# Kernel tuning notes

Hardware: AMD Instinct MI355X
Metric: run time of the kernel (lower is better)

The kernel has to match this reference:

```python
import jax, jax.numpy as jnp
from jax import lax
import numpy as np

DN = ('NCHW', 'OIHW', 'NCHW')

def conv(x, w, b, stride, pad):
    y = lax.conv_general_dilated(x, w, (stride, stride), [(pad, pad), (pad, pad)], dimension_numbers=DN)
    return y if b is None else y + b[None, :, None, None]

def conv_transpose(x, w, b):
    # torch ConvTranspose2d(k=4, s=2, p=1); w in torch layout (Cin, Cout, 4, 4)
    w_f = jnp.flip(w, (2, 3)).transpose(1, 0, 2, 3)  # -> OIHW, flipped
    y = lax.conv_general_dilated(x, w_f, (1, 1), [(2, 2), (2, 2)], lhs_dilation=(2, 2), dimension_numbers=DN)
    return y + b[None, :, None, None]

def res_stack(x, w3, w1, n_layers=2):
    # shared weights across layers (ModuleList([layer]*n) aliases one module)
    for _ in range(n_layers):
        h = conv(jax.nn.relu(x), w3, None, 1, 1)
        h = conv(jax.nn.relu(h), w1, None, 1, 0)
        x = x + h
    return jax.nn.relu(x)

def setup_inputs() -> dict:
    key = jax.random.key(0)
    ks = jax.random.split(key, 16)
    s = 0.02
    d = {
        'x': jax.random.normal(ks[0], (32, 3, 256, 256), jnp.float32),
        'enc_w1': jax.random.normal(ks[1], (128, 3, 4, 4), jnp.float32) * s,
        'enc_b1': jnp.zeros((128,), jnp.float32),
        'enc_w2': jax.random.normal(ks[2], (256, 128, 4, 4), jnp.float32) * s,
        'enc_b2': jnp.zeros((256,), jnp.float32),
        'enc_w3': jax.random.normal(ks[3], (512, 256, 4, 4), jnp.float32) * s,
        'enc_b3': jnp.zeros((512,), jnp.float32),
        'enc_res_w3': jax.random.normal(ks[4], (32, 512, 3, 3), jnp.float32) * s,
        'enc_res_w1': jax.random.normal(ks[5], (512, 32, 1, 1), jnp.float32) * s,
        'prevq_w': jax.random.normal(ks[6], (64, 512, 1, 1), jnp.float32) * s,
        'prevq_b': jnp.zeros((64,), jnp.float32),
        'emb': jax.random.normal(ks[7], (512, 64), jnp.float32),
        'dec_w1': jax.random.normal(ks[8], (64, 256, 4, 4), jnp.float32) * s,
        'dec_b1': jnp.zeros((256,), jnp.float32),
        'dec_res_w3': jax.random.normal(ks[9], (32, 256, 3, 3), jnp.float32) * s,
        'dec_res_w1': jax.random.normal(ks[10], (256, 32, 1, 1), jnp.float32) * s,
        'dec_w2': jax.random.normal(ks[11], (256, 128, 4, 4), jnp.float32) * s,
        'dec_b2': jnp.zeros((128,), jnp.float32),
        'dec_w3': jax.random.normal(ks[12], (128, 3, 4, 4), jnp.float32) * s,
        'dec_b3': jnp.zeros((3,), jnp.float32),
    }
    return d

def vqvae_fwd(x, enc_w1, enc_b1, enc_w2, enc_b2, enc_w3, enc_b3, enc_res_w3, enc_res_w1,
              prevq_w, prevq_b, emb, dec_w1, dec_b1, dec_res_w3, dec_res_w1,
              dec_w2, dec_b2, dec_w3, dec_b3):
    # encoder
    z = jax.nn.relu(conv(x, enc_w1, enc_b1, 2, 1))
    z = jax.nn.relu(conv(z, enc_w2, enc_b2, 2, 1))
    z = conv(z, enc_w3, enc_b3, 2, 1)
    z = res_stack(z, enc_res_w3, enc_res_w1)
    z_e = conv(z, prevq_w, prevq_b, 1, 0)  # (B, D=64, 32, 32)
    # vector quantiser
    B, C, H, W = z_e.shape
    x_flat = z_e.reshape(B, C, H * W).transpose(0, 2, 1)  # (B, HW, D)
    d2 = (jnp.sum(x_flat ** 2, -1, keepdims=True)
          - 2.0 * jnp.einsum('bnd,kd->bnk', x_flat, emb)
          + jnp.sum(emb ** 2, -1))
    idx = jnp.argmin(d2, axis=2)  # (B, HW)
    z_q_flat = emb[idx]  # (B, HW, D)
    z_q = z_q_flat.transpose(0, 2, 1).reshape(B, C, H, W)
    sg = lax.stop_gradient
    q_loss = jnp.mean((sg(z_q_flat) - x_flat) ** 2) + jnp.mean((z_q_flat - sg(x_flat)) ** 2)
    # decoder
    y = conv_transpose(z_q, dec_w1, dec_b1)  # (B, 256, 64, 64)
    y = res_stack(y, dec_res_w3, dec_res_w1)
    y = jax.nn.relu(conv_transpose(y, dec_w2, dec_b2))
    y = conv_transpose(y, dec_w3, dec_b3)  # (B, 3, 256, 256)
    return y, q_loss

def reference(x, enc_w1, enc_b1, enc_w2, enc_b2, enc_w3, enc_b3, enc_res_w3, enc_res_w1,
              prevq_w, prevq_b, emb, dec_w1, dec_b1, dec_res_w3, dec_res_w1,
              dec_w2, dec_b2, dec_w3, dec_b3):
    return vqvae_fwd(x, enc_w1, enc_b1, enc_w2, enc_b2, enc_w3, enc_b3, enc_res_w3, enc_res_w1,
                     prevq_w, prevq_b, emb, dec_w1, dec_b1, dec_res_w3, dec_res_w1,
                     dec_w2, dec_b2, dec_w3, dec_b3)
```

## Files before the change

### kernel.cpp

```cpp
#include <hip/hip_runtime.h>
#include <hip/hip_bf16.h>

typedef __attribute__((ext_vector_type(8))) short short8;
typedef __attribute__((ext_vector_type(4))) float f32x4;
typedef __attribute__((ext_vector_type(4))) unsigned int uint4v;

__device__ __forceinline__ unsigned short f2bf(float f) {
  unsigned u = __builtin_bit_cast(unsigned, f);
  u = (u + 0x7FFFu + ((u >> 16) & 1u)) >> 16;
  return (unsigned short)u;
}
__device__ __forceinline__ float bf2f(unsigned short h) {
  unsigned u = ((unsigned)h) << 16;
  return __builtin_bit_cast(float, u);
}
__device__ __forceinline__ unsigned pk_bf16(float a, float b) {
  __hip_bfloat162 h = __float22bfloat162_rn(make_float2(a, b));
  unsigned u;
  __builtin_memcpy(&u, &h, 4);
  return u;
}

template<int TMT, int MT, int MODE, int ZSP, bool SPLIT, bool RELU_IN, bool RELU_OUT, bool BIAS, int SM>
__global__ __launch_bounds__(256, (MT == 4) ? 3 : 4) void k_mfconv(
    const float* __restrict__ in, const unsigned short* __restrict__ wp,
    const float* __restrict__ bias, float* __restrict__ out,
    int Ci, int inW, int inH, int pWSH, int pHWSH,
    int Co, int ntap, int ntt,
    unsigned syp, unsigned sxp,
    int outW, int outHW, int CoSt) {
  const int tid  = threadIdx.x;
  const int lane = tid & 63, wave = tid >> 6;
  const int pW  = 1 << pWSH;
  const int pHW = 1 << pHWSH;
  const int inHW = inW * inH;
  const int nk32 = Ci >> 5;
  const int KS   = (nk32 >= 2) ? 2 : 1;
  const int NITS = 4 * KS;
  const int cpt  = nk32 / KS;
  const int total = ntap * cpt;
  constexpr int TT = TMT * MT;

  int bx = blockIdx.x;
  const int gx = gridDim.x;
  if ((gx & 7) == 0) bx = (bx & 7) * (gx >> 3) + (bx >> 3);
  const int n0  = bx * 64;
  const int coG = blockIdx.y;
  const int ph  = (MODE == 1) ? blockIdx.z : 0;
  const int tap0 = (MODE == 1) ? ph * 4 : 0;
  const int pdy = ph >> 1, pdx = ph & 1;

  int it0 = 0, itEnd = total;
  if (MODE != 1 && ZSP > 1) {
    const int per = total / ZSP;
    it0 = blockIdx.z * per;
    itEnd = it0 + per;
  }

  constexpr int NPL = SPLIT ? 2 : 1;
  constexpr int PL = 64 * 70;
  __shared__ __align__(16) unsigned short Bs[2 * NPL * PL];

  const int px  = lane;
  const int p   = n0 + px;
  const int img = p >> pHWSH;
  const int rem = p & (pHW - 1);
  const int y   = rem >> pWSH;
  const int x   = rem & (pW - 1);
  const size_t base_img = (size_t)img * Ci * inHW;

  constexpr int NTO = (TMT == 4) ? 4 : 2;
  const int mt0 = (TMT == 4) ? wave : (wave & 1);
  const int ntb = (TMT == 4) ? 0 : ((wave >> 1) * 2);
  f32x4 acc[MT * NTO];
#pragma unroll
  for (int u = 0; u < MT * NTO; ++u) acc[u] = (f32x4){0.f, 0.f, 0.f, 0.f};

  const int cp = wave;
  float v[16];

  auto ldr = [&](int tap_, int chunk_) {
    const int T = tap0 + tap_;
    const int dy = (int)((syp >> (2 * T)) & 3u) - 1;
    const int dx = (int)((sxp >> (2 * T)) & 3u) - 1;
    const int ys = (MODE == 2) ? (2 * y + dy) : (y + dy);
    const int xs = (MODE == 2) ? (2 * x + dx) : (x + dx);
    const bool ok = ((unsigned)ys < (unsigned)inH) && ((unsigned)xs < (unsigned)inW);
    const float* __restrict__ ipb = in + base_img + (ptrdiff_t)ys * inW + xs;
    const int ci0 = chunk_ * (KS * 32);
#pragma unroll
    for (int it2 = 0; it2 < 8; ++it2) {
      if (it2 >= NITS) break;
      const int cl = 2 * (cp + 4 * it2);
      float a = 0.f, b = 0.f;
      if (ok) {
        a = ipb[(size_t)(ci0 + cl) * inHW];
        b = ipb[(size_t)(ci0 + cl + 1) * inHW];
      }
      if (RELU_IN) { a = fmaxf(a, 0.f); b = fmaxf(b, 0.f); }
      v[2 * it2] = a; v[2 * it2 + 1] = b;
    }
  };
  auto pwr = [&](int b) {
#pragma unroll
    for (int it2 = 0; it2 < 8; ++it2) {
      if (it2 >= NITS) break;
      const int cl = 2 * (cp + 4 * it2);
      float a = v[2 * it2], c = v[2 * it2 + 1];
      unsigned hp = pk_bf16(a, c);
      *(unsigned*)&Bs[(b * NPL) * PL + px * 70 + cl] = hp;
      if (SPLIT) {
        float h0 = bf2f((unsigned short)hp), h1 = bf2f((unsigned short)(hp >> 16));
        *(unsigned*)&Bs[(b * NPL + 1) * PL + px * 70 + cl] = pk_bf16(a - h0, c - h1);
      }
    }
  };

  int tap = it0 / cpt, chunk = it0 % cpt;
  ldr(tap, chunk);
  pwr(0);
  __syncthreads();

  for (int it = it0; it < itEnd; ++it) {
    const int b = (it - it0) & 1;
    const int T = tap0 + tap;
    int tap2 = tap, chunk2 = chunk + 1;
    if (chunk2 == cpt) { chunk2 = 0; tap2 = tap + 1; }
    const bool more = (it + 1 < itEnd);
    if (more) ldr(tap2, chunk2);
#pragma unroll
    for (int s = 0; s < 2; ++s) {
      if (s >= KS) break;
      const int cic = chunk * KS + s;
      short8 ah[MT], al[MT];
#pragma unroll
      for (int m = 0; m < MT; ++m) {
        const int mtm = mt0 + m * TMT;
        size_t abase;
        if (SPLIT) abase = ((((size_t)coG * ntt + T) * nk32 + cic) * 2 * TT + mtm) * 512;
        else       abase = ((((size_t)coG * ntt + T) * nk32 + cic) * TT + mtm) * 512;
        ah[m] = *(const short8*)(wp + abase + (size_t)lane * 8);
        if (SPLIT) al[m] = *(const short8*)(wp + abase + (size_t)TT * 512 + (size_t)lane * 8);
      }
      short8 bh[NTO], bl[NTO];
#pragma unroll
      for (int u = 0; u < NTO; ++u) {
        const int row = 16 * (ntb + u) + (lane & 15);
        const unsigned* bp = (const unsigned*)&Bs[(b * NPL) * PL + row * 70 + s * 32 + (lane >> 4) * 8];
        uint4v hv = {bp[0], bp[1], bp[2], bp[3]};
        bh[u] = __builtin_bit_cast(short8, hv);
        if (SPLIT) {
          const unsigned* bpl = bp + (PL >> 1);
          uint4v lv = {bpl[0], bpl[1], bpl[2], bpl[3]};
          bl[u] = __builtin_bit_cast(short8, lv);
        }
      }
#pragma unroll
      for (int m = 0; m < MT; ++m)
#pragma unroll
        for (int u = 0; u < NTO; ++u) {
          f32x4 a = acc[m * NTO + u];
          a = __builtin_amdgcn_mfma_f32_16x16x32_bf16(ah[m], bh[u], a, 0, 0, 0);
          if (SPLIT) {
            a = __builtin_amdgcn_mfma_f32_16x16x32_bf16(al[m], bh[u], a, 0, 0, 0);
            a = __builtin_amdgcn_mfma_f32_16x16x32_bf16(ah[m], bl[u], a, 0, 0, 0);
          }
          acc[m * NTO + u] = a;
        }
    }
    if (more) {
      pwr(b ^ 1);
      __syncthreads();
    }
    tap = tap2; chunk = chunk2;
  }

#pragma unroll
  for (int m = 0; m < MT; ++m) {
    const int mtm = mt0 + m * TMT;
#pragma unroll
    for (int u = 0; u < NTO; ++u) {
      const int nt = ntb + u;
      const int pn = n0 + nt * 16 + (lane & 15);
      const int img2 = pn >> pHWSH;
      const int rem2 = pn & (pHW - 1);
      const int y2 = rem2 >> pWSH, x2 = rem2 & (pW - 1);
      int oy, ox;
      if (MODE == 1) { oy = 2 * y2 + pdy; ox = 2 * x2 + pdx; }
      else           { oy = y2;           ox = x2; }
#pragma unroll
      for (int r = 0; r < 4; ++r) {
        const int co = coG * (TT * 16) + mtm * 16 + (lane >> 4) * 4 + r;
        if (co < CoSt) {
          float val = acc[m * NTO + u][r];
          if (BIAS) val += bias[co];
          if (RELU_OUT) val = fmaxf(val, 0.f);
          size_t oi = ((size_t)img2 * Co + co) * outHW + (size_t)oy * outW + ox;
          if (SM == 0) out[oi] = val;
          else if (SM == 1) out[oi] += val;
          else atomicAdd(&out[oi], val);
        }
      }
    }
  }
}

template<int MGRP, bool SPLIT>
__global__ __launch_bounds__(256, SPLIT ? 3 : 4) void k_mfres(
    const float* __restrict__ in, const unsigned short* __restrict__ w3p,
    const unsigned short* __restrict__ w1p, float* __restrict__ znew,
    int pWSH, int pHWSH, unsigned syp, unsigned sxp) {
  constexpr int C = MGRP * 64;
  const int tid = threadIdx.x, lane = tid & 63, wave = tid >> 6;
  const int pW = 1 << pWSH, pHW = 1 << pHWSH;
  const int inW = pW, inH = pHW >> pWSH;
  const int inHW = pHW;
  const int nk32 = C >> 5;
  const int cpt = nk32 >> 1;
  const int total = 9 * cpt;

  int bx = blockIdx.x;
  const int gx = gridDim.x;
  if ((gx & 7) == 0) bx = (bx & 7) * (gx >> 3) + (bx >> 3);
  const int n0 = bx * 64;

  constexpr int NPL = SPLIT ? 2 : 1;
  constexpr int PL = 64 * 70;
  __shared__ __align__(16) unsigned short Bs[2 * NPL * PL];
  __shared__ __align__(16) unsigned short Hs2[NPL * 2560];

  const int px = lane;
  const int p = n0 + px;
  const int img = p >> pHWSH;
  const int rem = p & (pHW - 1);
  const int y = rem >> pWSH, x = rem & (pW - 1);
  const size_t base_img = (size_t)img * C * inHW;
  const int mt = wave & 1, ntb = (wave >> 1) * 2;
  const int cp = wave;
  float v[16];
  f32x4 acc[2];
  acc[0] = (f32x4){0.f, 0.f, 0.f, 0.f};
  acc[1] = (f32x4){0.f, 0.f, 0.f, 0.f};

  auto ldr = [&](int T, int chunk_) {
    const int dy = (int)((syp >> (2 * T)) & 3u) - 1;
    const int dx = (int)((sxp >> (2 * T)) & 3u) - 1;
    const int ys = y + dy, xs = x + dx;
    const bool ok = ((unsigned)ys < (unsigned)inH) && ((unsigned)xs < (unsigned)inW);
    const float* __restrict__ ipb = in + base_img + (ptrdiff_t)ys * inW + xs;
    const int ci0 = chunk_ * 64;
#pragma unroll
    for (int i2 = 0; i2 < 8; ++i2) {
      const int cl = 2 * (cp + 4 * i2);
      float a = 0.f, b = 0.f;
      if (ok) {
        a = ipb[(size_t)(ci0 + cl) * inHW];
        b = ipb[(size_t)(ci0 + cl + 1) * inHW];
      }
      a = fmaxf(a, 0.f); b = fmaxf(b, 0.f);
      v[2 * i2] = a; v[2 * i2 + 1] = b;
    }
  };
  auto pwr = [&](int b) {
#pragma unroll
    for (int i2 = 0; i2 < 8; ++i2) {
      const int cl = 2 * (cp + 4 * i2);
      float a = v[2 * i2], c = v[2 * i2 + 1];
      unsigned hp = pk_bf16(a, c);
      *(unsigned*)&Bs[(b * NPL) * PL + px * 70 + cl] = hp;
      if (SPLIT) {
        float h0 = bf2f((unsigned short)hp), h1 = bf2f((unsigned short)(hp >> 16));
        *(unsigned*)&Bs[(b * NPL + 1) * PL + px * 70 + cl] = pk_bf16(a - h0, c - h1);
      }
    }
  };

  int tap = 0, chunk = 0;
  ldr(0, 0);
  pwr(0);
  __syncthreads();
  for (int it = 0; it < total; ++it) {
    const int b = it & 1;
    const int T = tap;
    int tap2 = tap, chunk2 = chunk + 1;
    if (chunk2 == cpt) { chunk2 = 0; tap2 = tap + 1; }
    const bool more = (it + 1 < total);
    if (more) ldr(tap2, chunk2);
#pragma unroll
    for (int s = 0; s < 2; ++s) {
      const int cic = chunk * 2 + s;
      size_t abase;
      if (SPLIT) abase = (((size_t)T * nk32 + cic) * 2 * 2 + mt) * 512;
      else       abase = (((size_t)T * nk32 + cic) * 2 + mt) * 512;
      short8 ah = *(const short8*)(w3p + abase + (size_t)lane * 8);
      short8 al;
      if (SPLIT) al = *(const short8*)(w3p + abase + 2 * 512 + (size_t)lane * 8);
#pragma unroll
      for (int u = 0; u < 2; ++u) {
        const int row = 16 * (ntb + u) + (lane & 15);
        const unsigned* bp = (const unsigned*)&Bs[(b * NPL) * PL + row * 70 + s * 32 + (lane >> 4) * 8];
        uint4v hv = {bp[0], bp[1], bp[2], bp[3]};
        short8 bh = __builtin_bit_cast(short8, hv);
        f32x4 a = acc[u];
        a = __builtin_amdgcn_mfma_f32_16x16x32_bf16(ah, bh, a, 0, 0, 0);
        if (SPLIT) {
          const unsigned* bpl = bp + (PL >> 1);
          uint4v lv = {bpl[0], bpl[1], bpl[2], bpl[3]};
          short8 bl = __builtin_bit_cast(short8, lv);
          a = __builtin_amdgcn_mfma_f32_16x16x32_bf16(al, bh, a, 0, 0, 0);
          a = __builtin_amdgcn_mfma_f32_16x16x32_bf16(ah, bl, a, 0, 0, 0);
        }
        acc[u] = a;
      }
    }
    if (more) {
      pwr(b ^ 1);
      __syncthreads();
    }
    tap = tap2; chunk = chunk2;
  }

#pragma unroll
  for (int u = 0; u < 2; ++u) {
    const int pxl = (ntb + u) * 16 + (lane & 15);
#pragma unroll
    for (int r = 0; r < 4; ++r) {
      const int co = mt * 16 + (lane >> 4) * 4 + r;
      float val = fmaxf(acc[u][r], 0.f);
      unsigned short hv = f2bf(val);
      Hs2[pxl * 40 + co] = hv;
      if (SPLIT) Hs2[2560 + pxl * 40 + co] = f2bf(val - bf2f(hv));
    }
  }
  __syncthreads();

  short8 bh2[4], bl2[4];
#pragma unroll
  for (int u = 0; u < 4; ++u) {
    const int row = 16 * u + (lane & 15);
    bh2[u] = *(const short8*)&Hs2[row * 40 + (lane >> 4) * 8];
    if (SPLIT) bl2[u] = *(const short8*)&Hs2[2560 + row * 40 + (lane >> 4) * 8];
  }
#pragma unroll
  for (int g = 0; g < MGRP; ++g) {
    const int mt2 = wave + 4 * g;
    short8 a1h = *(const short8*)(w1p + (size_t)mt2 * 512 + (size_t)lane * 8);
    short8 a1l;
    if (SPLIT) a1l = *(const short8*)(w1p + ((size_t)(MGRP * 4) + mt2) * 512 + (size_t)lane * 8);
    f32x4 a2[4];
#pragma unroll
    for (int u = 0; u < 4; ++u) a2[u] = (f32x4){0.f, 0.f, 0.f, 0.f};
#pragma unroll
    for (int u = 0; u < 4; ++u) {
      a2[u] = __builtin_amdgcn_mfma_f32_16x16x32_bf16(a1h, bh2[u], a2[u], 0, 0, 0);
      if (SPLIT) {
        a2[u] = __builtin_amdgcn_mfma_f32_16x16x32_bf16(a1l, bh2[u], a2[u], 0, 0, 0);
        a2[u] = __builtin_amdgcn_mfma_f32_16x16x32_bf16(a1h, bl2[u], a2[u], 0, 0, 0);
      }
    }
#pragma unroll
    for (int u = 0; u < 4; ++u) {
      const int pn = n0 + u * 16 + (lane & 15);
      const int rem2 = pn & (pHW - 1);
#pragma unroll
      for (int r = 0; r < 4; ++r) {
        const int co = mt2 * 16 + (lane >> 4) * 4 + r;
        size_t oi = ((size_t)img * C + co) * inHW + rem2;
        znew[oi] = in[oi] + a2[u][r];
      }
    }
  }
}

__global__ __launch_bounds__(256, 4) void k_mfenc1(
    const float* __restrict__ in, const unsigned short* __restrict__ wp,
    const float* __restrict__ bias, float* __restrict__ out) {
  const int tid = threadIdx.x, lane = tid & 63, wave = tid >> 6;
  int bx = blockIdx.x;
  const int gx = gridDim.x;
  if ((gx & 7) == 0) bx = (bx & 7) * (gx >> 3) + (bx >> 3);
  const int n0 = bx * 64;
  const int p = n0 + lane;
  const int img = p >> 14;
  const int rem = p & 16383;
  const int y = rem >> 7, x = rem & 127;
  __shared__ __align__(16) unsigned short Bs[2 * 4480];
  const float* __restrict__ ib = in + (size_t)img * 3 * 65536;
#pragma unroll
  for (int i = 0; i < 8; ++i) {
    const int kk0 = 2 * (wave + 4 * i);
    float vv[2];
#pragma unroll
    for (int q = 0; q < 2; ++q) {
      const int kk = kk0 + q;
      const int tap = kk >> 2, c = kk & 3;
      const int iy = 2 * y + (tap >> 2) - 1, ix = 2 * x + (tap & 3) - 1;
      const bool ok = (c < 3) && ((unsigned)iy < 256u) && ((unsigned)ix < 256u);
      vv[q] = ok ? ib[((size_t)c << 16) + (size_t)iy * 256 + ix] : 0.f;
    }
    unsigned hp = pk_bf16(vv[0], vv[1]);
    *(unsigned*)&Bs[lane * 70 + kk0] = hp;
    float h0 = bf2f((unsigned short)hp), h1 = bf2f((unsigned short)(hp >> 16));
    *(unsigned*)&Bs[4480 + lane * 70 + kk0] = pk_bf16(vv[0] - h0, vv[1] - h1);
  }
  __syncthreads();

  f32x4 acc[8];
#pragma unroll
  for (int u = 0; u < 8; ++u) acc[u] = (f32x4){0.f, 0.f, 0.f, 0.f};
#pragma unroll
  for (int s = 0; s < 2; ++s) {
    short8 ah[2], al[2];
#pragma unroll
    for (int m = 0; m < 2; ++m) {
      const int mtm = wave + m * 4;
      size_t abase = (((size_t)s * 2 + 0) * 8 + mtm) * 512;
      ah[m] = *(const short8*)(wp + abase + (size_t)lane * 8);
      al[m] = *(const short8*)(wp + abase + 8 * 512 + (size_t)lane * 8);
    }
    short8 bh[4], bl[4];
#pragma unroll
    for (int u = 0; u < 4; ++u) {
      const int row = 16 * u + (lane & 15);
      const unsigned* bp = (const unsigned*)&Bs[row * 70 + s * 32 + (lane >> 4) * 8];
      uint4v hv = {bp[0], bp[1], bp[2], bp[3]};
      bh[u] = __builtin_bit_cast(short8, hv);
      const unsigned* bpl = bp + 2240;
      uint4v lv = {bpl[0], bpl[1], bpl[2], bpl[3]};
      bl[u] = __builtin_bit_cast(short8, lv);
    }
#pragma unroll
    for (int m = 0; m < 2; ++m)
#pragma unroll
      for (int u = 0; u < 4; ++u) {
        f32x4 a = acc[m * 4 + u];
        a = __builtin_amdgcn_mfma_f32_16x16x32_bf16(ah[m], bh[u], a, 0, 0, 0);
        a = __builtin_amdgcn_mfma_f32_16x16x32_bf16(al[m], bh[u], a, 0, 0, 0);
        a = __builtin_amdgcn_mfma_f32_16x16x32_bf16(ah[m], bl[u], a, 0, 0, 0);
        acc[m * 4 + u] = a;
      }
  }
#pragma unroll
  for (int m = 0; m < 2; ++m)
#pragma unroll
    for (int u = 0; u < 4; ++u) {
      const int pn = n0 + u * 16 + (lane & 15);
      const int img2 = pn >> 14;
      const int rem2 = pn & 16383;
#pragma unroll
      for (int r = 0; r < 4; ++r) {
        const int co = (wave + m * 4) * 16 + (lane >> 4) * 4 + r;
        float val = fmaxf(acc[m * 4 + u][r] + bias[co], 0.f);
        out[((size_t)img2 * 128 + co) * 16384 + rem2] = val;
      }
    }
}

template<bool SPLIT>
__global__ __launch_bounds__(256) void k_pack_o(
    const float* __restrict__ w, unsigned short* __restrict__ p,
    int Co, int Ci, int ntap, int TMT, int E) {
  int i = blockIdx.x * 256 + threadIdx.x;
  if (i >= E) return;
  const int NC = Ci >> 5;
  int j = i & 7, lane = (i >> 3) & 63, r = i >> 9;
  int mt = r % TMT; r /= TMT;
  int sp = 0;
  if (SPLIT) { sp = r % 2; r /= 2; }
  int cic = r % NC; r /= NC;
  int T = r % ntap; int coG = r / ntap;
  int co = coG * (TMT * 16) + mt * 16 + (lane & 15);
  int ci = cic * 32 + (lane >> 4) * 8 + j;
  float wv = w[((size_t)co * Ci + ci) * ntap + T];
  unsigned short hv = f2bf(wv);
  p[i] = (SPLIT && sp == 1) ? f2bf(wv - bf2f(hv)) : hv;
}

__global__ __launch_bounds__(256) void k_pack_ct(
    const float* __restrict__ w, unsigned short* __restrict__ p,
    int Ci, int CoR, int TMT, int E) {
  int i = blockIdx.x * 256 + threadIdx.x;
  if (i >= E) return;
  const int NC = Ci >> 5;
  int j = i & 7, lane = (i >> 3) & 63, r = i >> 9;
  int mt = r % TMT; r /= TMT;
  int cic = r % NC; r /= NC;
  int T = r % 16;   int coG = r / 16;
  int phx = T >> 2, t = T & 3;
  int dy = phx >> 1, dx = phx & 1, ty = t >> 1, tx = t & 1;
  int ky = 2 * ty + 1 - dy, kx = 2 * tx + 1 - dx;
  int co = coG * (TMT * 16) + mt * 16 + (lane & 15);
  int ci = cic * 32 + (lane >> 4) * 8 + j;
  float wv = (co < CoR) ? w[(((size_t)ci * CoR + co) * 4 + ky) * 4 + kx] : 0.f;
  p[i] = f2bf(wv);
}

__global__ __launch_bounds__(256) void k_pack_e1(
    const float* __restrict__ w, unsigned short* __restrict__ p) {
  int i = blockIdx.x * 256 + threadIdx.x;
  int j = i & 7, lane = (i >> 3) & 63, r = i >> 9;
  int mt = r % 8; r /= 8;
  int sp = r % 2; r /= 2;
  int cic = r;
  int co = mt * 16 + (lane & 15);
  int kk = cic * 32 + (lane >> 4) * 8 + j;
  int tap = kk >> 2, c = kk & 3;
  float wv = (c < 3) ? w[(((size_t)co * 3 + c) * 4 + (tap >> 2)) * 4 + (tap & 3)] : 0.f;
  unsigned short hv = f2bf(wv);
  p[i] = (sp == 1) ? f2bf(wv - bf2f(hv)) : hv;
}

template<int COB, bool RELU_OUT>
__global__ __launch_bounds__(256) void k_conv4(
    const float* __restrict__ in, const float* __restrict__ w,
    const float* __restrict__ bias, float* __restrict__ out,
    int N, int Ci, int Hi, int Wi, int Co) {
  const int Ho = Hi >> 1, Wo = Wi >> 1;
  const int ow = blockIdx.x * 16 + (threadIdx.x & 15);
  const int oh = blockIdx.y * 16 + (threadIdx.x >> 4);
  const int zcnt = Co / COB;
  const int co0 = (blockIdx.z % zcnt) * COB;
  const int n   = blockIdx.z / zcnt;
  if (oh >= Ho || ow >= Wo) return;
  const float* __restrict__ ip = in + (size_t)n * Ci * Hi * Wi;
  float acc[COB];
#pragma unroll
  for (int j = 0; j < COB; ++j) acc[j] = bias[co0 + j];
  const int ih0 = 2 * oh - 1, iw0 = 2 * ow - 1;
  for (int ci = 0; ci < Ci; ++ci) {
    const float* __restrict__ ic = ip + (size_t)ci * Hi * Wi;
    float v[16];
#pragma unroll
    for (int kh = 0; kh < 4; ++kh) {
      const int ih = ih0 + kh;
      const bool hok = (unsigned)ih < (unsigned)Hi;
      const float* __restrict__ irow = ic + (long)ih * Wi;
#pragma unroll
      for (int kw = 0; kw < 4; ++kw) {
        const int iw = iw0 + kw;
        v[kh * 4 + kw] = (hok && (unsigned)iw < (unsigned)Wi) ? irow[iw] : 0.f;
      }
    }
#pragma unroll
    for (int j = 0; j < COB; ++j) {
      const float* __restrict__ wc = w + ((size_t)(co0 + j) * Ci + ci) * 16;
#pragma unroll
      for (int t = 0; t < 16; ++t) acc[j] = fmaf(v[t], wc[t], acc[j]);
    }
  }
#pragma unroll
  for (int j = 0; j < COB; ++j) {
    float a = acc[j];
    if (RELU_OUT) a = fmaxf(a, 0.f);
    out[(((size_t)n * Co + co0 + j) * Ho + oh) * Wo + ow] = a;
  }
}

template<int COB, bool RELU_IN, int CSPLIT>
__global__ __launch_bounds__(256) void k_conv3(
    const float* __restrict__ in, const float* __restrict__ w,
    float* __restrict__ out, int N, int Ci, int H, int W, int Co) {
  const int ow = blockIdx.x * 16 + (threadIdx.x & 15);
  const int oh = blockIdx.y * 16 + (threadIdx.x >> 4);
  const int zcnt = Co / COB;
  const int z = blockIdx.z;
  const int cs  = z % CSPLIT;
  const int co0 = ((z / CSPLIT) % zcnt) * COB;
  const int n   = z / (CSPLIT * zcnt);
  if (oh >= H || ow >= W) return;
  const int CPS = Ci / CSPLIT;
  const float* __restrict__ ip = in + (size_t)n * Ci * H * W;
  float acc[COB];
#pragma unroll
  for (int j = 0; j < COB; ++j) acc[j] = 0.f;
  for (int ci = cs * CPS; ci < (cs + 1) * CPS; ++ci) {
    const float* __restrict__ ic = ip + (size_t)ci * H * W;
    float v[9];
#pragma unroll
    for (int kh = 0; kh < 3; ++kh) {
      const int ih = oh - 1 + kh;
      const bool hok = (unsigned)ih < (unsigned)H;
      const float* __restrict__ irow = ic + (long)ih * W;
#pragma unroll
      for (int kw = 0; kw < 3; ++kw) {
        const int iw = ow - 1 + kw;
        float t = (hok && (unsigned)iw < (unsigned)W) ? irow[iw] : 0.f;
        if (RELU_IN) t = fmaxf(t, 0.f);
        v[kh * 3 + kw] = t;
      }
    }
#pragma unroll
    for (int j = 0; j < COB; ++j) {
      const float* __restrict__ wc = w + ((size_t)(co0 + j) * Ci + ci) * 9;
#pragma unroll
      for (int t = 0; t < 9; ++t) acc[j] = fmaf(v[t], wc[t], acc[j]);
    }
  }
#pragma unroll
  for (int j = 0; j < COB; ++j) {
    size_t oi = (((size_t)n * Co + co0 + j) * H + oh) * W + ow;
    if (CSPLIT > 1) atomicAdd(&out[oi], acc[j]);
    else out[oi] = acc[j];
  }
}

template<int COB, bool RELU_IN, bool ACCUM>
__global__ __launch_bounds__(256) void k_conv1(
    const float* __restrict__ in, const float* __restrict__ w,
    const float* __restrict__ bias, float* __restrict__ out,
    int N, int Ci, int P, int Co) {
  const int p = blockIdx.x * 256 + threadIdx.x;
  const int co0 = blockIdx.y * COB;
  const int n = blockIdx.z;
  if (p >= P) return;
  float acc[COB];
#pragma unroll
  for (int j = 0; j < COB; ++j) acc[j] = bias ? bias[co0 + j] : 0.f;
  const float* __restrict__ ip = in + (size_t)n * Ci * P + p;
#pragma unroll 8
  for (int ci = 0; ci < Ci; ++ci) {
    float v = ip[(size_t)ci * P];
    if (RELU_IN) v = fmaxf(v, 0.f);
#pragma unroll
    for (int j = 0; j < COB; ++j)
      acc[j] = fmaf(v, w[(size_t)(co0 + j) * Ci + ci], acc[j]);
  }
#pragma unroll
  for (int j = 0; j < COB; ++j) {
    size_t oi = ((size_t)n * Co + co0 + j) * P + p;
    if (ACCUM) out[oi] += acc[j]; else out[oi] = acc[j];
  }
}

template<int COB, bool RELU_IN, bool RELU_OUT>
__global__ __launch_bounds__(256) void k_convT(
    const float* __restrict__ in, const float* __restrict__ w,
    const float* __restrict__ bias, float* __restrict__ out,
    int N, int Ci, int Hi, int Wi, int Co) {
  const int Ho = Hi * 2, Wo = Wi * 2;
  const int x = blockIdx.x * 16 + (threadIdx.x & 15);
  const int y = blockIdx.y * 16 + (threadIdx.x >> 4);
  const int zcnt = Co / COB;
  const int co0 = (blockIdx.z % zcnt) * COB;
  const int n   = blockIdx.z / zcnt;
  if (x >= Wi || y >= Hi) return;
  const float* __restrict__ ip = in + (size_t)n * Ci * Hi * Wi;
  float a00[COB], a01[COB], a10[COB], a11[COB];
#pragma unroll
  for (int j = 0; j < COB; ++j) {
    float b = bias[co0 + j];
    a00[j] = b; a01[j] = b; a10[j] = b; a11[j] = b;
  }
  const bool r0 = y > 0, r2 = y + 1 < Hi, c0 = x > 0, c2 = x + 1 < Wi;
#pragma unroll 2
  for (int ci = 0; ci < Ci; ++ci) {
    const float* __restrict__ ic = ip + (size_t)ci * Hi * Wi + (size_t)y * Wi + x;
    float v00 = 0.f, v01 = 0.f, v02 = 0.f, v10 = 0.f, v12 = 0.f,
          v20 = 0.f, v21 = 0.f, v22 = 0.f;
    float v11 = ic[0];
    if (c0) v10 = ic[-1];
    if (c2) v12 = ic[1];
    if (r0) { v01 = ic[-Wi]; if (c0) v00 = ic[-Wi - 1]; if (c2) v02 = ic[-Wi + 1]; }
    if (r2) { v21 = ic[Wi];  if (c0) v20 = ic[Wi - 1];  if (c2) v22 = ic[Wi + 1]; }
    if (RELU_IN) {
      v00 = fmaxf(v00, 0.f); v01 = fmaxf(v01, 0.f); v02 = fmaxf(v02, 0.f);
      v10 = fmaxf(v10, 0.f); v11 = fmaxf(v11, 0.f); v12 = fmaxf(v12, 0.f);
      v20 = fmaxf(v20, 0.f); v21 = fmaxf(v21, 0.f); v22 = fmaxf(v22, 0.f);
    }
#pragma unroll
    for (int j = 0; j < COB; ++j) {
      const float* __restrict__ wc = w + ((size_t)ci * Co + co0 + j) * 16;
      a00[j] = fmaf(v11, wc[5],  fmaf(v10, wc[7],  fmaf(v01, wc[13], fmaf(v00, wc[15], a00[j]))));
      a01[j] = fmaf(v12, wc[4],  fmaf(v11, wc[6],  fmaf(v02, wc[12], fmaf(v01, wc[14], a01[j]))));
      a10[j] = fmaf(v21, wc[1],  fmaf(v20, wc[3],  fmaf(v11, wc[9],  fmaf(v10, wc[11], a10[j]))));
      a11[j] = fmaf(v22, wc[0],  fmaf(v21, wc[2],  fmaf(v12, wc[8],  fmaf(v11, wc[10], a11[j]))));
    }
  }
#pragma unroll
  for (int j = 0; j < COB; ++j) {
    size_t b = ((size_t)n * Co + co0 + j) * Ho;
    float o00 = a00[j], o01 = a01[j], o10 = a10[j], o11 = a11[j];
    if (RELU_OUT) {
      o00 = fmaxf(o00, 0.f); o01 = fmaxf(o01, 0.f);
      o10 = fmaxf(o10, 0.f); o11 = fmaxf(o11, 0.f);
    }
    out[(b + 2 * y) * Wo + 2 * x]         = o00;
    out[(b + 2 * y) * Wo + 2 * x + 1]     = o01;
    out[(b + 2 * y + 1) * Wo + 2 * x]     = o10;
    out[(b + 2 * y + 1) * Wo + 2 * x + 1] = o11;
  }
}

__global__ __launch_bounds__(256, 2) void k_vq(
    const float* __restrict__ ze, const float* __restrict__ emb,
    const float* __restrict__ qb,
    float* __restrict__ zq, float* __restrict__ loss) {
  __shared__ float e2s[512];
  const int tid = threadIdx.x;
  for (int k = tid; k < 512; k += 256) {
    const f32x4* e4 = (const f32x4*)(emb + (size_t)k * 64);
    float s = 0.f;
#pragma unroll
    for (int dq = 0; dq < 16; ++dq) {
      f32x4 ev = e4[dq];
      s = fmaf(ev[0], ev[0], s); s = fmaf(ev[1], ev[1], s);
      s = fmaf(ev[2], ev[2], s); s = fmaf(ev[3], ev[3], s);
    }
    e2s[k] = s;
  }
  __syncthreads();
  const int p = blockIdx.x * 256 + tid;
  const int n = p >> 10, px = p & 1023;
  float xv[64];
  const float* __restrict__ zp = ze + (size_t)n * 64 * 1024 + px;
#pragma unroll
  for (int d = 0; d < 64; ++d) xv[d] = zp[(size_t)d * 1024] + (qb ? qb[d] : 0.f);
  float best = 1e30f; int bi = 0;
  for (int k = 0; k < 512; ++k) {
    const f32x4* e4 = (const f32x4*)(emb + (size_t)k * 64);
    float dot = 0.f;
#pragma unroll
    for (int dq = 0; dq < 16; ++dq) {
      f32x4 ev = e4[dq];
      dot = fmaf(xv[4 * dq],     ev[0], dot);
      dot = fmaf(xv[4 * dq + 1], ev[1], dot);
      dot = fmaf(xv[4 * dq + 2], ev[2], dot);
      dot = fmaf(xv[4 * dq + 3], ev[3], dot);
    }
    float sc = fmaf(-2.f, dot, e2s[k]);
    if (sc < best) { best = sc; bi = k; }
  }
  const float* __restrict__ eb = emb + (size_t)bi * 64;
  float* __restrict__ qp = zq + (size_t)n * 64 * 1024 + px;
  float l = 0.f;
#pragma unroll
  for (int d = 0; d < 64; ++d) {
    float ev = eb[d];
    qp[(size_t)d * 1024] = ev;
    float df = ev - xv[d];
    l = fmaf(df, df, l);
  }
#pragma unroll
  for (int off = 32; off > 0; off >>= 1) l += __shfl_down(l, off, 64);
  if ((tid & 63) == 0) atomicAdd(loss, l * (2.f / 2097152.f));
}

__global__ __launch_bounds__(64) void k_vq64(
    const float* __restrict__ ze, const float* __restrict__ emb,
    float* __restrict__ zq, float* __restrict__ loss,
    int N, int P, int K) {
  const int t = blockIdx.x * 64 + threadIdx.x;
  if (t >= N * P) return;
  const int n = t / P, p = t % P;
  float xv[64];
  const float* __restrict__ zp = ze + (size_t)n * 64 * P + p;
#pragma unroll
  for (int d = 0; d < 64; ++d) xv[d] = zp[(size_t)d * P];
  float best = 1e30f; int bi = 0;
  for (int k = 0; k < K; ++k) {
    const float* __restrict__ e = emb + (size_t)k * 64;
    float dot = 0.f, e2 = 0.f;
#pragma unroll
    for (int d = 0; d < 64; ++d) {
      float ev = e[d];
      dot = fmaf(xv[d], ev, dot);
      e2  = fmaf(ev, ev, e2);
    }
    float score = e2 - 2.f * dot;
    if (score < best) { best = score; bi = k; }
  }
  const float* __restrict__ eb = emb + (size_t)bi * 64;
  float* __restrict__ qp = zq + (size_t)n * 64 * P + p;
  float l = 0.f;
#pragma unroll
  for (int d = 0; d < 64; ++d) {
    float ev = eb[d];
    qp[(size_t)d * P] = ev;
    float df = ev - xv[d];
    l = fmaf(df, df, l);
  }
#pragma unroll
  for (int off = 32; off > 0; off >>= 1) l += __shfl_down(l, off, 64);
  if ((threadIdx.x & 63) == 0) atomicAdd(loss, l * (2.f / 2097152.f));
}

extern "C" void kernel_launch(void* const* d_in, const int* in_sizes, int n_in,
                              void* d_out, int out_size, void* d_ws, size_t ws_size,
                              hipStream_t stream) {
  const float* x    = (const float*)d_in[0];
  const float* ew1  = (const float*)d_in[1];
  const float* eb1  = (const float*)d_in[2];
  const float* ew2  = (const float*)d_in[3];
  const float* eb2  = (const float*)d_in[4];
  const float* ew3  = (const float*)d_in[5];
  const float* eb3  = (const float*)d_in[6];
  const float* erw3 = (const float*)d_in[7];
  const float* erw1 = (const float*)d_in[8];
  const float* pqw  = (const float*)d_in[9];
  const float* pqb  = (const float*)d_in[10];
  const float* emb  = (const float*)d_in[11];
  const float* dw1  = (const float*)d_in[12];
  const float* db1  = (const float*)d_in[13];
  const float* drw3 = (const float*)d_in[14];
  const float* drw1 = (const float*)d_in[15];
  const float* dw2  = (const float*)d_in[16];
  const float* db2  = (const float*)d_in[17];
  const float* dw3  = (const float*)d_in[18];
  const float* db3  = (const float*)d_in[19];
  float* out = (float*)d_out;
  char*  ws  = (char*)d_ws;
  float* loss = out + 6291456;
  const size_t MiB = 1048576ull, KiB = 1024ull;

  dim3 blk(256);
  hipMemsetAsync(loss, 0, 4, stream);

  unsigned syct = 0, sxct = 0;
  for (int T = 0; T < 16; ++T) {
    int phx = T >> 2, dy = phx >> 1, dx = phx & 1, t = T & 3, ty = t >> 1, tx = t & 1;
    int sy = (dy == 0) ? (ty ? -1 : 0) : (ty ? 0 : 1);
    int sx = (dx == 0) ? (tx ? -1 : 0) : (tx ? 0 : 1);
    syct |= (unsigned)(sy + 1) << (2 * T);
    sxct |= (unsigned)(sx + 1) << (2 * T);
  }
  unsigned syc3 = 0, sxc3 = 0;
  for (int t = 0; t < 9; ++t) {
    syc3 |= (unsigned)(t / 3) << (2 * t);
    sxc3 |= (unsigned)(t % 3) << (2 * t);
  }
  unsigned syc4 = 0, sxc4 = 0;
  for (int t = 0; t < 16; ++t) {
    syc4 |= (unsigned)(t / 4) << (2 * t);
    sxc4 |= (unsigned)(t % 4) << (2 * t);
  }
  const unsigned sy1 = 1, sx1 = 1;

  auto packs = [&](char* PB) {
    unsigned short* e2p   = (unsigned short*)(PB);
    unsigned short* e3p   = (unsigned short*)(PB + 2048 * KiB);
    unsigned short* erc3p = (unsigned short*)(PB + 10240 * KiB);
    unsigned short* erc1p = (unsigned short*)(PB + 10816 * KiB);
    unsigned short* pqp   = (unsigned short*)(PB + 10880 * KiB);
    unsigned short* d1p   = (unsigned short*)(PB + 11008 * KiB);
    unsigned short* d2p   = (unsigned short*)(PB + 11520 * KiB);
    unsigned short* dc3p  = (unsigned short*)(PB + 12544 * KiB);
    unsigned short* dc1p  = (unsigned short*)(PB + 12688 * KiB);
    unsigned short* e1p   = (unsigned short*)(PB + 12704 * KiB);
    unsigned short* d3p   = (unsigned short*)(PB + 12832 * KiB);
    unsigned short* erc1F = (unsigned short*)(PB + 12960 * KiB);
    unsigned short* dc1F  = (unsigned short*)(PB + 13024 * KiB);
    k_pack_o<true ><<<dim3(1048576 / 256), blk, 0, stream>>>(ew2,  e2p,  256, 128, 16, 8, 1048576);
    k_pack_o<true ><<<dim3(4194304 / 256), blk, 0, stream>>>(ew3,  e3p,  512, 256, 16, 8, 4194304);
    k_pack_o<true ><<<dim3(294912 / 256),  blk, 0, stream>>>(erw3, erc3p, 32, 512,  9, 2, 294912);
    k_pack_o<true ><<<dim3(32768 / 256),   blk, 0, stream>>>(erw1, erc1p, 512, 32,  1, 8, 32768);
    k_pack_o<true ><<<dim3(65536 / 256),   blk, 0, stream>>>(pqw,  pqp,   64, 512,  1, 4, 65536);
    k_pack_ct<<<dim3(262144 / 256), blk, 0, stream>>>(dw1, d1p, 64, 256, 16, 262144);
    k_pack_ct<<<dim3(524288 / 256), blk, 0, stream>>>(dw2, d2p, 256, 128, 8, 524288);
    k_pack_o<false><<<dim3(73728 / 256),   blk, 0, stream>>>(drw3, dc3p,  32, 256,  9, 2, 73728);
    k_pack_o<false><<<dim3(8192 / 256),    blk, 0, stream>>>(drw1, dc1p, 256, 32,  1, 8, 8192);
    k_pack_e1<<<dim3(256), blk, 0, stream>>>(ew1, e1p);
    k_pack_ct<<<dim3(65536 / 256), blk, 0, stream>>>(dw3, d3p, 128, 3, 2, 65536);
    k_pack_o<true ><<<dim3(32768 / 256), blk, 0, stream>>>(erw1, erc1F, 512, 32, 1, 32, 32768);
    k_pack_o<false><<<dim3(8192 / 256),  blk, 0, stream>>>(drw1, dc1F, 256, 32, 1, 16, 8192);
  };

  if (ws_size >= 498ull * MiB) {
    float* z1  = (float*)ws;
    float* z2  = (float*)(ws + 256 * MiB);
    float* z3  = (float*)(ws + 384 * MiB);
    float* z3b = (float*)ws;
    float* ze  = (float*)(ws + 452 * MiB);
    float* zq  = (float*)(ws + 460 * MiB);
    char*  PB  = ws + 484 * MiB;
    unsigned short* e2p   = (unsigned short*)(PB);
    unsigned short* e3p   = (unsigned short*)(PB + 2048 * KiB);
    unsigned short* erc3p = (unsigned short*)(PB + 10240 * KiB);
    unsigned short* pqp   = (unsigned short*)(PB + 10880 * KiB);
    unsigned short* d1p   = (unsigned short*)(PB + 11008 * KiB);
    unsigned short* d2p   = (unsigned short*)(PB + 11520 * KiB);
    unsigned short* dc3p  = (unsigned short*)(PB + 12544 * KiB);
    unsigned short* e1p   = (unsigned short*)(PB + 12704 * KiB);
    unsigned short* d3p   = (unsigned short*)(PB + 12832 * KiB);
    unsigned short* erc1F = (unsigned short*)(PB + 12960 * KiB);
    unsigned short* dc1F  = (unsigned short*)(PB + 13024 * KiB);
    packs(PB);

    k_mfenc1<<<dim3(8192), blk, 0, stream>>>(x, e1p, eb1, z1);
    k_mfconv<4, 2, 2, 1, true, false, true, true, 0><<<dim3(2048, 2), blk, 0, stream>>>(
        z1, e2p, eb2, z2, 128, 128, 128, 6, 12, 256, 16, 16, syc4, sxc4, 64, 4096, 256);
    k_mfconv<4, 2, 2, 1, true, false, false, true, 0><<<dim3(512, 4), blk, 0, stream>>>(
        z2, e3p, eb3, z3, 256, 64, 64, 5, 10, 512, 16, 16, syc4, sxc4, 32, 1024, 512);
    k_mfres<8, true><<<dim3(512), blk, 0, stream>>>(z3,  erc3p, erc1F, z3b, 5, 10, syc3, sxc3);
    k_mfres<8, true><<<dim3(512), blk, 0, stream>>>(z3b, erc3p, erc1F, z3,  5, 10, syc3, sxc3);
    k_mfconv<4, 1, 0, 1, true, true, false, false, 0><<<dim3(512, 1), blk, 0, stream>>>(
        z3, pqp, nullptr, ze, 512, 32, 32, 5, 10, 64, 1, 1, sy1, sx1, 32, 1024, 64);
    k_vq<<<dim3(128), blk, 0, stream>>>(ze, emb, pqb, zq, loss);
    float* y1  = (float*)(ws + 256 * MiB);
    float* y1b = (float*)ws;
    float* y2  = (float*)ws;
    k_mfconv<4, 4, 1, 1, false, false, false, true, 0><<<dim3(512, 1, 4), blk, 0, stream>>>(
        zq, d1p, db1, y1, 64, 32, 32, 5, 10, 256, 4, 16, syct, sxct, 64, 4096, 256);
    k_mfres<4, false><<<dim3(2048), blk, 0, stream>>>(y1,  dc3p, dc1F, y1b, 6, 12, syc3, sxc3);
    k_mfres<4, false><<<dim3(2048), blk, 0, stream>>>(y1b, dc3p, dc1F, y1,  6, 12, syc3, sxc3);
    k_mfconv<4, 2, 1, 1, false, true, true, true, 0><<<dim3(2048, 1, 4), blk, 0, stream>>>(
        y1, d2p, db2, y2, 256, 64, 64, 6, 12, 128, 4, 16, syct, sxct, 128, 16384, 128);
    k_mfconv<2, 1, 1, 1, false, false, false, true, 0><<<dim3(8192, 1, 4), blk, 0, stream>>>(
        y2, d3p, db3, out, 128, 128, 128, 7, 14, 3, 4, 16, syct, sxct, 256, 65536, 3);
    return;
  }

  if (ws_size >= 128ull * MiB) {
    float* z3  = (float*)ws;
    float* h   = (float*)(ws + 64 * MiB);
    float* ze  = (float*)(ws + 68 * MiB);
    float* zq  = (float*)(ws + 100 * MiB);
    char*  PB  = ws + 115 * MiB;
    unsigned short* e2p   = (unsigned short*)(PB);
    unsigned short* e3p   = (unsigned short*)(PB + 2048 * KiB);
    unsigned short* erc3p = (unsigned short*)(PB + 10240 * KiB);
    unsigned short* erc1p = (unsigned short*)(PB + 10816 * KiB);
    unsigned short* pqp   = (unsigned short*)(PB + 10880 * KiB);
    unsigned short* d1p   = (unsigned short*)(PB + 11008 * KiB);
    unsigned short* d2p   = (unsigned short*)(PB + 11520 * KiB);
    unsigned short* dc3p  = (unsigned short*)(PB + 12544 * KiB);
    unsigned short* dc1p  = (unsigned short*)(PB + 12688 * KiB);
    unsigned short* e1p   = (unsigned short*)(PB + 12704 * KiB);
    unsigned short* d3p   = (unsigned short*)(PB + 12832 * KiB);
    packs(PB);

    const int NE = 4;
    float* z1c = (float*)(ws + 64 * MiB);
    float* z2c = (float*)(ws + 96 * MiB);
    for (int n0 = 0; n0 < 32; n0 += NE) {
      const float* xb = x + (size_t)n0 * 3 * 65536;
      float* z3b2 = z3 + (size_t)n0 * 512 * 1024;
      k_mfenc1<<<dim3(NE * 256), blk, 0, stream>>>(xb, e1p, eb1, z1c);
      k_mfconv<4, 2, 2, 1, true, false, true, true, 0><<<dim3(256, 2), blk, 0, stream>>>(
          z1c, e2p, eb2, z2c, 128, 128, 128, 6, 12, 256, 16, 16, syc4, sxc4, 64, 4096, 256);
      k_mfconv<4, 2, 2, 1, true, false, false, true, 0><<<dim3(64, 4), blk, 0, stream>>>(
          z2c, e3p, eb3, z3b2, 256, 64, 64, 5, 10, 512, 16, 16, syc4, sxc4, 32, 1024, 512);
    }
    for (int i = 0; i < 2; ++i) {
      hipMemsetAsync(h, 0, 4 * MiB, stream);
      k_mfconv<2, 1, 0, 3, true, true, false, false, 2><<<dim3(512, 1, 3), blk, 0, stream>>>(
          z3, erc3p, nullptr, h, 512, 32, 32, 5, 10, 32, 9, 9, syc3, sxc3, 32, 1024, 32);
      k_mfconv<4, 2, 0, 1, true, true, false, false, 1><<<dim3(512, 4), blk, 0, stream>>>(
          h, erc1p, nullptr, z3, 32, 32, 32, 5, 10, 512, 1, 1, sy1, sx1, 32, 1024, 512);
    }
    k_mfconv<4, 1, 0, 1, true, true, false, false, 0><<<dim3(512, 1), blk, 0, stream>>>(
        z3, pqp, nullptr, ze, 512, 32, 32, 5, 10, 64, 1, 1, sy1, sx1, 32, 1024, 64);
    k_vq<<<dim3(128), blk, 0, stream>>>(ze, emb, pqb, zq, loss);

    const int ND = 8;
    float* y1c = (float*)ws;
    float* hd  = (float*)(ws + 32 * MiB);
    float* y2c = (float*)(ws + 36 * MiB);
    for (int c = 0; c < 32; c += ND) {
      const float* zqb = zq + (size_t)c * 64 * 1024;
      float* outb = out + (size_t)c * 3 * 65536;
      k_mfconv<4, 4, 1, 1, false, false, false, true, 0><<<dim3(128, 1, 4), blk, 0, stream>>>(
          zqb, d1p, db1, y1c, 64, 32, 32, 5, 10, 256, 4, 16, syct, sxct, 64, 4096, 256);
      for (int i = 0; i < 2; ++i) {
        hipMemsetAsync(hd, 0, 4 * MiB, stream);
        k_mfconv<2, 1, 0, 3, false, true, false, false, 2><<<dim3(512, 1, 3), blk, 0, stream>>>(
            y1c, dc3p, nullptr, hd, 256, 64, 64, 6, 12, 32, 9, 9, syc3, sxc3, 64, 4096, 32);
        k_mfconv<4, 2, 0, 1, false, true, false, false, 1><<<dim3(512, 2), blk, 0, stream>>>(
            hd, dc1p, nullptr, y1c, 32, 64, 64, 6, 12, 256, 1, 1, sy1, sx1, 64, 4096, 256);
      }
      k_mfconv<4, 2, 1, 1, false, true, true, true, 0><<<dim3(512, 1, 4), blk, 0, stream>>>(
          y1c, d2p, db2, y2c, 256, 64, 64, 6, 12, 128, 4, 16, syct, sxct, 128, 16384, 128);
      k_mfconv<2, 1, 1, 1, false, false, false, true, 0><<<dim3(2048, 1, 4), blk, 0, stream>>>(
          y2c, d3p, db3, outb, 128, 128, 128, 7, 14, 3, 4, 16, syct, sxct, 256, 65536, 3);
    }
    return;
  }

  const size_t PER_IMG = 12582912ull;
  int NB = (int)(ws_size / PER_IMG);
  if (NB > 32) NB = 32;
  if (NB < 1)  NB = 1;

  for (int n0 = 0; n0 < 32; n0 += NB) {
    const int nb = (32 - n0 < NB) ? (32 - n0) : NB;
    const float* xb   = x   + (size_t)n0 * 3 * 65536;
    float*       outb = out + (size_t)n0 * 3 * 65536;

    float* z1 = (float*)ws;
    float* z2 = (float*)(ws + (size_t)NB * 8388608ull);
    float* z3 = (float*)ws;
    char*  tb = ws + (size_t)NB * 2097152ull;
    float* he = (float*)tb;
    float* ze = (float*)(tb + (size_t)NB * 131072ull);
    float* zq = (float*)(tb + (size_t)NB * 393216ull);
    float* hd = (float*)(tb + (size_t)NB * 655360ull);
    float* y1 = z2;
    float* y2 = (float*)ws;

    k_conv4<4, true ><<<dim3(8, 8, nb * 32), blk, 0, stream>>>(xb, ew1, eb1, z1, nb,   3, 256, 256, 128);
    k_conv4<4, true ><<<dim3(4, 4, nb * 64), blk, 0, stream>>>(z1, ew2, eb2, z2, nb, 128, 128, 128, 256);
    k_conv4<4, false><<<dim3(2, 2, nb * 128), blk, 0, stream>>>(z2, ew3, eb3, z3, nb, 256,  64,  64, 512);
    for (int i = 0; i < 2; ++i) {
      k_conv3<4, true, 1><<<dim3(2, 2, nb * 8), blk, 0, stream>>>(z3, erw3, he, nb, 512, 32, 32, 32);
      k_conv1<8, true, true><<<dim3(4, 64, nb), blk, 0, stream>>>(he, erw1, nullptr, z3, nb, 32, 1024, 512);
    }
    k_conv1<8, true, false><<<dim3(4, 8, nb), blk, 0, stream>>>(z3, pqw, pqb, ze, nb, 512, 1024, 64);
    k_vq64<<<dim3(nb * 16), dim3(64), 0, stream>>>(ze, emb, zq, loss, nb, 1024, 512);
    k_convT<4, false, false><<<dim3(2, 2, nb * 64), blk, 0, stream>>>(zq, dw1, db1, y1, nb,  64, 32, 32, 256);
    for (int i = 0; i < 2; ++i) {
      k_conv3<4, true, 1><<<dim3(4, 4, nb * 8), blk, 0, stream>>>(y1, drw3, hd, nb, 256, 64, 64, 32);
      k_conv1<8, true, true><<<dim3(16, 32, nb), blk, 0, stream>>>(hd, drw1, nullptr, y1, nb, 32, 4096, 256);
    }
    k_convT<4, true, true ><<<dim3(4, 4, nb * 32), blk, 0, stream>>>(y1, dw2, db2, y2, nb, 256, 64, 64, 128);
    k_convT<1, false, false><<<dim3(8, 8, nb * 3), blk, 0, stream>>>(y2, dw3, db3, outb, nb, 128, 128, 128, 3);
  }
}
```

Baseline: 4.148 ms.

## Fuse four transposed-conv output phases into one kernel sharing input tiles

Adds a k_mfct kernel that computes all four output parity phases of the stride-2 transposed convolutions in one block. It iterates over the 3x3 set of input shifts and routes each loaded input tile to every phase/tap that uses that shift, where before a separate grid z-slice handled each phase. The dec2/dec3 transposed convs use this kernel, so input activations are loaded and converted once instead of once per phase. The dec1 conv now uses a smaller M tile with more co groups, and the weight pack group parameter changes to match. The fused kernel holds four phases of accumulators, which raises register pressure and may lower occupancy.

```diff
diff --git a/kernel.cpp b/kernel.cpp
--- a/kernel.cpp
+++ b/kernel.cpp
@@ -199,6 +199,143 @@
           if (SM == 0) out[oi] = val;
           else if (SM == 1) out[oi] += val;
           else atomicAdd(&out[oi], val);
+        }
+      }
+    }
+  }
+}
+
+template<int TMT, bool RELU_IN, bool RELU_OUT>
+__global__ __launch_bounds__(256, (TMT == 4) ? 3 : 4) void k_mfct(
+    const float* __restrict__ in, const unsigned short* __restrict__ wp,
+    const float* __restrict__ bias, float* __restrict__ out,
+    int Ci, int inW, int inH, int pWSH, int pHWSH, int Co, int CoSt) {
+  const int tid = threadIdx.x, lane = tid & 63, wave = tid >> 6;
+  const int pW = 1 << pWSH, pHW = 1 << pHWSH;
+  const int inHW = inW * inH;
+  const int nk32 = Ci >> 5;
+  const int cpt = nk32 >> 1;
+  const int total = 9 * cpt;
+
+  int bx = blockIdx.x;
+  const int gx = gridDim.x;
+  if ((gx & 7) == 0) bx = (bx & 7) * (gx >> 3) + (bx >> 3);
+  const int n0 = bx * 64;
+  const int coG = blockIdx.y;
+
+  constexpr int PL = 64 * 70;
+  __shared__ __align__(16) unsigned short Bs[2 * PL];
+
+  const int px = lane;
+  const int p = n0 + px;
+  const int img = p >> pHWSH;
+  const int rem = p & (pHW - 1);
+  const int y = rem >> pWSH, x = rem & (pW - 1);
+  const size_t base_img = (size_t)img * Ci * inHW;
+
+  constexpr int NTO = (TMT == 4) ? 4 : 2;
+  const int mt0 = (TMT == 4) ? wave : (wave & 1);
+  const int ntb = (TMT == 4) ? 0 : ((wave >> 1) * 2);
+  f32x4 acc[4 * NTO];
+#pragma unroll
+  for (int u = 0; u < 4 * NTO; ++u) acc[u] = (f32x4){0.f, 0.f, 0.f, 0.f};
+
+  const int cp = wave;
+  float v[16];
+
+  auto ldr = [&](int st, int chunk_) {
+    const int sy = st / 3 - 1, sx = st % 3 - 1;
+    const int ys = y + sy, xs = x + sx;
+    const bool ok = ((unsigned)ys < (unsigned)inH) && ((unsigned)xs < (unsigned)inW);
+    const float* __restrict__ ipb = in + base_img + (ptrdiff_t)ys * inW + xs;
+    const int ci0 = chunk_ * 64;
+#pragma unroll
+    for (int i2 = 0; i2 < 8; ++i2) {
+      const int cl = 2 * (cp + 4 * i2);
+      float a = 0.f, b = 0.f;
+      if (ok) {
+        a = ipb[(size_t)(ci0 + cl) * inHW];
+        b = ipb[(size_t)(ci0 + cl + 1) * inHW];
+      }
+      if (RELU_IN) { a = fmaxf(a, 0.f); b = fmaxf(b, 0.f); }
+      v[2 * i2] = a; v[2 * i2 + 1] = b;
+    }
+  };
+  auto pwr = [&](int b) {
+#pragma unroll
+    for (int i2 = 0; i2 < 8; ++i2) {
+      const int cl = 2 * (cp + 4 * i2);
+      *(unsigned*)&Bs[b * PL + px * 70 + cl] = pk_bf16(v[2 * i2], v[2 * i2 + 1]);
+    }
+  };
+
+  int st = 0, chunk = 0;
+  ldr(0, 0);
+  pwr(0);
+  __syncthreads();
+
+  for (int it = 0; it < total; ++it) {
+    const int b = it & 1;
+    const int sy = st / 3 - 1, sx = st % 3 - 1;
+    int st2 = st, chunk2 = chunk + 1;
+    if (chunk2 == cpt) { chunk2 = 0; st2 = st + 1; }
+    const bool more = (it + 1 < total);
+    if (more) ldr(st2, chunk2);
+#pragma unroll
+    for (int s = 0; s < 2; ++s) {
+      const int cic = chunk * 2 + s;
+      short8 bh[NTO];
+#pragma unroll
+      for (int u = 0; u < NTO; ++u) {
+        const int row = 16 * (ntb + u) + (lane & 15);
+        bh[u] = *(const short8*)&Bs[b * PL + row * 70 + s * 32 + (lane >> 4) * 8];
+      }
+#pragma unroll
+      for (int dy = 0; dy < 2; ++dy)
+#pragma unroll
+        for (int ty = 0; ty < 2; ++ty)
+#pragma unroll
+          for (int dx = 0; dx < 2; ++dx)
+#pragma unroll
+            for (int tx = 0; tx < 2; ++tx) {
+              const int csy = (dy == 0) ? (ty ? -1 : 0) : (ty ? 0 : 1);
+              const int csx = (dx == 0) ? (tx ? -1 : 0) : (tx ? 0 : 1);
+              if (csy != sy || csx != sx) continue;
+              constexpr int phc = 0;  (void)phc;
+              const int T = (dy * 2 + dx) * 4 + ty * 2 + tx;
+              size_t abase = ((((size_t)coG * 16 + T) * nk32 + cic) * TMT + mt0) * 512;
+              short8 ah = *(const short8*)(wp + abase + (size_t)lane * 8);
+#pragma unroll
+              for (int u = 0; u < NTO; ++u) {
+                acc[(dy * 2 + dx) * NTO + u] = __builtin_amdgcn_mfma_f32_16x16x32_bf16(
+                    ah, bh[u], acc[(dy * 2 + dx) * NTO + u], 0, 0, 0);
+              }
+            }
+    }
+    if (more) {
+      pwr(b ^ 1);
+      __syncthreads();
+    }
+    st = st2; chunk = chunk2;
+  }
+
+  const int outW = 2 * pW, outHW = 4 * pHW;
+#pragma unroll
+  for (int u = 0; u < NTO; ++u) {
+    const int pn = n0 + (ntb + u) * 16 + (lane & 15);
+    const int img2 = pn >> pHWSH;
+    const int rem2 = pn & (pHW - 1);
+    const int y2 = rem2 >> pWSH, x2 = rem2 & (pW - 1);
+#pragma unroll
+    for (int ph = 0; ph < 4; ++ph) {
+      const int oy = 2 * y2 + (ph >> 1), ox = 2 * x2 + (ph & 1);
+#pragma unroll
+      for (int r = 0; r < 4; ++r) {
+        const int co = coG * (TMT * 16) + mt0 * 16 + (lane >> 4) * 4 + r;
+        if (co < CoSt) {
+          float val = acc[ph * NTO + u][r] + bias[co];
+          if (RELU_OUT) val = fmaxf(val, 0.f);
+          out[((size_t)img2 * Co + co) * outHW + (size_t)oy * outW + ox] = val;
         }
       }
     }
@@ -854,8 +991,8 @@
     k_pack_o<true ><<<dim3(294912 / 256),  blk, 0, stream>>>(erw3, erc3p, 32, 512,  9, 2, 294912);
     k_pack_o<true ><<<dim3(32768 / 256),   blk, 0, stream>>>(erw1, erc1p, 512, 32,  1, 8, 32768);
     k_pack_o<true ><<<dim3(65536 / 256),   blk, 0, stream>>>(pqw,  pqp,   64, 512,  1, 4, 65536);
-    k_pack_ct<<<dim3(262144 / 256), blk, 0, stream>>>(dw1, d1p, 64, 256, 16, 262144);
-    k_pack_ct<<<dim3(524288 / 256), blk, 0, stream>>>(dw2, d2p, 256, 128, 8, 524288);
+    k_pack_ct<<<dim3(262144 / 256), blk, 0, stream>>>(dw1, d1p, 64, 256, 8, 262144);
+    k_pack_ct<<<dim3(524288 / 256), blk, 0, stream>>>(dw2, d2p, 256, 128, 4, 524288);
     k_pack_o<false><<<dim3(73728 / 256),   blk, 0, stream>>>(drw3, dc3p,  32, 256,  9, 2, 73728);
     k_pack_o<false><<<dim3(8192 / 256),    blk, 0, stream>>>(drw1, dc1p, 256, 32,  1, 8, 8192);
     k_pack_e1<<<dim3(256), blk, 0, stream>>>(ew1, e1p);
@@ -898,14 +1035,14 @@
     float* y1  = (float*)(ws + 256 * MiB);
     float* y1b = (float*)ws;
     float* y2  = (float*)ws;
-    k_mfconv<4, 4, 1, 1, false, false, false, true, 0><<<dim3(512, 1, 4), blk, 0, stream>>>(
+    k_mfconv<4, 2, 1, 1, false, false, false, true, 0><<<dim3(512, 2, 4), blk, 0, stream>>>(
         zq, d1p, db1, y1, 64, 32, 32, 5, 10, 256, 4, 16, syct, sxct, 64, 4096, 256);
     k_mfres<4, false><<<dim3(2048), blk, 0, stream>>>(y1,  dc3p, dc1F, y1b, 6, 12, syc3, sxc3);
     k_mfres<4, false><<<dim3(2048), blk, 0, stream>>>(y1b, dc3p, dc1F, y1,  6, 12, syc3, sxc3);
-    k_mfconv<4, 2, 1, 1, false, true, true, true, 0><<<dim3(2048, 1, 4), blk, 0, stream>>>(
-        y1, d2p, db2, y2, 256, 64, 64, 6, 12, 128, 4, 16, syct, sxct, 128, 16384, 128);
-    k_mfconv<2, 1, 1, 1, false, false, false, true, 0><<<dim3(8192, 1, 4), blk, 0, stream>>>(
-        y2, d3p, db3, out, 128, 128, 128, 7, 14, 3, 4, 16, syct, sxct, 256, 65536, 3);
+    k_mfct<4, true, true><<<dim3(2048, 2), blk, 0, stream>>>(
+        y1, d2p, db2, y2, 256, 64, 64, 6, 12, 128, 128);
+    k_mfct<2, false, false><<<dim3(8192, 1), blk, 0, stream>>>(
+        y2, d3p, db3, out, 128, 128, 128, 7, 14, 3, 3);
     return;
   }
 
@@ -958,7 +1095,7 @@
     for (int c = 0; c < 32; c += ND) {
       const float* zqb = zq + (size_t)c * 64 * 1024;
       float* outb = out + (size_t)c * 3 * 65536;
-      k_mfconv<4, 4, 1, 1, false, false, false, true, 0><<<dim3(128, 1, 4), blk, 0, stream>>>(
+      k_mfconv<4, 2, 1, 1, false, false, false, true, 0><<<dim3(128, 2, 4), blk, 0, stream>>>(
           zqb, d1p, db1, y1c, 64, 32, 32, 5, 10, 256, 4, 16, syct, sxct, 64, 4096, 256);
       for (int i = 0; i < 2; ++i) {
         hipMemsetAsync(hd, 0, 4 * MiB, stream);
@@ -967,10 +1104,10 @@
         k_mfconv<4, 2, 0, 1, false, true, false, false, 1><<<dim3(512, 2), blk, 0, stream>>>(
             hd, dc1p, nullptr, y1c, 32, 64, 64, 6, 12, 256, 1, 1, sy1, sx1, 64, 4096, 256);
       }
-      k_mfconv<4, 2, 1, 1, false, true, true, true, 0><<<dim3(512, 1, 4), blk, 0, stream>>>(
-          y1c, d2p, db2, y2c, 256, 64, 64, 6, 12, 128, 4, 16, syct, sxct, 128, 16384, 128);
-      k_mfconv<2, 1, 1, 1, false, false, false, true, 0><<<dim3(2048, 1, 4), blk, 0, stream>>>(
-          y2c, d3p, db3, outb, 128, 128, 128, 7, 14, 3, 4, 16, syct, sxct, 256, 65536, 3);
+      k_mfct<4, true, true><<<dim3(512, 2), blk, 0, stream>>>(
+          y1c, d2p, db2, y2c, 256, 64, 64, 6, 12, 128, 128);
+      k_mfct<2, false, false><<<dim3(2048, 1), blk, 0, stream>>>(
+          y2c, d3p, db3, outb, 128, 128, 128, 7, 14, 3, 3);
     }
     return;
   }
```

New measurement: 15.95 ms. 3.84x slower.
